# Kernel tuning notes

Hardware: AMD Instinct MI355X
Metric: run time of the kernel (lower is better)

Reference implementation:

```python
import jax, jax.numpy as jnp
import numpy as np

R = 5.0      # cutoff radius (init arg)
N = 4096     # total atoms
B = 8        # number of periodic systems in the batch


def setup_inputs() -> dict:
    key = jax.random.key(0)
    k1, k2, k3 = jax.random.split(key, 3)
    # positions in a ~20 Angstrom box (matches cell scale)
    pos = jax.random.uniform(k1, (N, 3), dtype=jnp.float32) * 20.0
    # sorted per-atom graph ids, as produced by a batched molecular loader
    batch = jnp.sort(jax.random.randint(k2, (N,), 0, B))
    # near-cubic 20A cells with small triclinic perturbation (well-conditioned)
    cell = jnp.eye(3, dtype=jnp.float32) * 20.0 + 0.5 * jax.random.normal(k3, (B, 3, 3), dtype=jnp.float32)
    return {"pos": pos, "cell": cell, "batch": batch}


def reference(pos, cell, batch):
    # Dense, fixed-shape equivalent of RadiusGraph.forward with PBC cell wrap.
    # Original returns dynamically filtered (edge_index, disp); here we return
    # the full [N,N,3] displacement grid (masked to 0 off-graph) plus the
    # boolean edge mask -- same math, jit-compatible static shapes.
    n = pos.shape[0]
    disp = pos[:, None, :] - pos[None, :, :]            # [N,N,3], row i minus col j
    # PBC minimum-image wrap: per edge, cell is taken from the ROW node's graph
    cell_n = cell[batch]                                # [N,3,3]
    inv_cellT = jnp.linalg.inv(jnp.swapaxes(cell_n, 1, 2))   # [N,3,3] = (cell^T)^{-1}
    # scaled = solve(cell^T, disp) vectorized over all pairs
    scaled = jnp.einsum('iab,ijb->ija', inv_cellT, disp)     # [N,N,3]
    disp = disp - jnp.einsum('iab,ijb->ija', cell_n, jnp.round(scaled))
    # edge validity: same graph, no self-loop, within cutoff (after wrap)
    same_graph = batch[:, None] == batch[None, :]
    not_self = ~jnp.eye(n, dtype=bool)
    mask = same_graph & not_self & (jnp.linalg.norm(disp, axis=-1) < R)
    disp = jnp.where(mask[..., None], disp, jnp.zeros((), disp.dtype))
    return disp, mask
```

## Files before the change

### kernel.cpp

```cpp
#include <hip/hip_runtime.h>
#include <math.h>

#define NATOMS 4096
#define R_CUT 5.0f
#define JPT 4
#define BLOCK 256
#define JPB (BLOCK * JPT)
#define IPB 8

typedef float f3 __attribute__((ext_vector_type(3), aligned(4)));

__global__ __launch_bounds__(BLOCK) void radius_graph_kernel(
    const float* __restrict__ pos,
    const float* __restrict__ cell,
    const int*   __restrict__ batch,
    float* __restrict__ disp_out,
    float* __restrict__ mask_out)
{
    const int bid = blockIdx.x;
    const int rg  = bid >> 2;
    const int jc  = bid & 3;
    const int tid = (int)threadIdx.x;

    float pjx[JPT], pjy[JPT], pjz[JPT];
    int   bj[JPT];
    #pragma unroll
    for (int k = 0; k < JPT; ++k) {
        const int j = jc * JPB + k * BLOCK + tid;
        pjx[k] = pos[j * 3 + 0];
        pjy[k] = pos[j * 3 + 1];
        pjz[k] = pos[j * 3 + 2];
        bj[k]  = batch[j];
    }

    const int i0 = rg * IPB;

    #pragma unroll 1
    for (int r = 0; r < IPB; ++r) {
        const int i = i0 + r;

        const int bi = batch[i];
        const float pix = pos[i * 3 + 0];
        const float piy = pos[i * 3 + 1];
        const float piz = pos[i * 3 + 2];

        const float* C = cell + (size_t)bi * 9;
        const float C00 = C[0], C01 = C[1], C02 = C[2];
        const float C10 = C[3], C11 = C[4], C12 = C[5];
        const float C20 = C[6], C21 = C[7], C22 = C[8];
        const float cof00 =  (C11 * C22 - C12 * C21);
        const float cof01 = -(C10 * C22 - C12 * C20);
        const float cof02 =  (C10 * C21 - C11 * C20);
        const float cof10 = -(C01 * C22 - C02 * C21);
        const float cof11 =  (C00 * C22 - C02 * C20);
        const float cof12 = -(C00 * C21 - C01 * C20);
        const float cof20 =  (C01 * C12 - C02 * C11);
        const float cof21 = -(C00 * C12 - C02 * C10);
        const float cof22 =  (C00 * C11 - C01 * C10);
        const float det = C00 * cof00 + C01 * cof01 + C02 * cof02;
        const float id  = 1.0f / det;
        const float A00 = cof00 * id, A01 = cof01 * id, A02 = cof02 * id;
        const float A10 = cof10 * id, A11 = cof11 * id, A12 = cof12 * id;
        const float A20 = cof20 * id, A21 = cof21 * id, A22 = cof22 * id;

        const size_t rowm = (size_t)i * NATOMS;
        const size_t rowd = rowm * 3;

        #pragma unroll
        for (int k = 0; k < JPT; ++k) {
            const int j = jc * JPB + k * BLOCK + tid;
            const float d0 = __fsub_rn(pix, pjx[k]);
            const float d1 = __fsub_rn(piy, pjy[k]);
            const float d2 = __fsub_rn(piz, pjz[k]);

            const float s0 = __fadd_rn(__fadd_rn(__fmul_rn(A00, d0), __fmul_rn(A01, d1)), __fmul_rn(A02, d2));
            const float s1 = __fadd_rn(__fadd_rn(__fmul_rn(A10, d0), __fmul_rn(A11, d1)), __fmul_rn(A12, d2));
            const float s2 = __fadd_rn(__fadd_rn(__fmul_rn(A20, d0), __fmul_rn(A21, d1)), __fmul_rn(A22, d2));

            const float r0 = rintf(s0);
            const float r1 = rintf(s1);
            const float r2 = rintf(s2);

            const float w0 = __fsub_rn(d0, __fadd_rn(__fadd_rn(__fmul_rn(C00, r0), __fmul_rn(C01, r1)), __fmul_rn(C02, r2)));
            const float w1 = __fsub_rn(d1, __fadd_rn(__fadd_rn(__fmul_rn(C10, r0), __fmul_rn(C11, r1)), __fmul_rn(C12, r2)));
            const float w2 = __fsub_rn(d2, __fadd_rn(__fadd_rn(__fmul_rn(C20, r0), __fmul_rn(C21, r1)), __fmul_rn(C22, r2)));

            const float n2 = __fadd_rn(__fadd_rn(__fmul_rn(w0, w0), __fmul_rn(w1, w1)), __fmul_rn(w2, w2));
            const bool m = (bi == bj[k]) && (i != j) && (sqrtf(n2) < R_CUT);

            f3 v;
            v.x = m ? w0 : 0.0f;
            v.y = m ? w1 : 0.0f;
            v.z = m ? w2 : 0.0f;
            *(f3*)(disp_out + rowd + (size_t)j * 3) = v;
            mask_out[rowm + (size_t)j] = m ? 1.0f : 0.0f;
        }
    }
}

extern "C" void kernel_launch(void* const* d_in, const int* in_sizes, int n_in,
                              void* d_out, int out_size, void* d_ws, size_t ws_size,
                              hipStream_t stream) {
    const float* pos   = (const float*)d_in[0];
    const float* cell  = (const float*)d_in[1];
    const int*   batch = (const int*)d_in[2];

    float* disp_out = (float*)d_out;
    float* mask_out = (float*)d_out + (size_t)NATOMS * NATOMS * 3;

    const int blocks = (NATOMS / IPB) * (NATOMS / JPB);
    radius_graph_kernel<<<blocks, BLOCK, 0, stream>>>(pos, cell, batch, disp_out, mask_out);
}
```

Measured before the change: 261.7 us.

## Switch to grid-stride persistent loop over contiguous row tiles

Replaces the fixed 2048-block grid, where each block owned 8 rows by 1024 columns, with a persistent grid of 2048 blocks looping over 256-wide row tiles. Each iteration writes one fully contiguous 256-element chunk of the output, so consecutive blocks stream adjacent memory. The trade-off is that j-atom positions are no longer kept in registers across rows, and the cell inverse is recomputed for every tile, adding loads and ALU work to a store-bound kernel.

```diff
diff --git a/kernel.cpp b/kernel.cpp
--- a/kernel.cpp
+++ b/kernel.cpp
@@ -3,10 +3,10 @@
 
 #define NATOMS 4096
 #define R_CUT 5.0f
-#define JPT 4
 #define BLOCK 256
-#define JPB (BLOCK * JPT)
-#define IPB 8
+#define GRID 2048
+#define TPR (NATOMS / BLOCK)
+#define NTILE (NATOMS * TPR)
 
 typedef float f3 __attribute__((ext_vector_type(3), aligned(4)));
 
@@ -17,27 +17,12 @@
     float* __restrict__ disp_out,
     float* __restrict__ mask_out)
 {
-    const int bid = blockIdx.x;
-    const int rg  = bid >> 2;
-    const int jc  = bid & 3;
     const int tid = (int)threadIdx.x;
 
-    float pjx[JPT], pjy[JPT], pjz[JPT];
-    int   bj[JPT];
-    #pragma unroll
-    for (int k = 0; k < JPT; ++k) {
-        const int j = jc * JPB + k * BLOCK + tid;
-        pjx[k] = pos[j * 3 + 0];
-        pjy[k] = pos[j * 3 + 1];
-        pjz[k] = pos[j * 3 + 2];
-        bj[k]  = batch[j];
-    }
-
-    const int i0 = rg * IPB;
-
-    #pragma unroll 1
-    for (int r = 0; r < IPB; ++r) {
-        const int i = i0 + r;
+    for (int T = (int)blockIdx.x; T < NTILE; T += GRID) {
+        const int i  = T >> 4;
+        const int jb = T & (TPR - 1);
+        const int j  = jb * BLOCK + tid;
 
         const int bi = batch[i];
         const float pix = pos[i * 3 + 0];
@@ -63,38 +48,36 @@
         const float A10 = cof10 * id, A11 = cof11 * id, A12 = cof12 * id;
         const float A20 = cof20 * id, A21 = cof21 * id, A22 = cof22 * id;
 
-        const size_t rowm = (size_t)i * NATOMS;
-        const size_t rowd = rowm * 3;
+        const float pjx = pos[j * 3 + 0];
+        const float pjy = pos[j * 3 + 1];
+        const float pjz = pos[j * 3 + 2];
+        const int   bjv = batch[j];
 
-        #pragma unroll
-        for (int k = 0; k < JPT; ++k) {
-            const int j = jc * JPB + k * BLOCK + tid;
-            const float d0 = __fsub_rn(pix, pjx[k]);
-            const float d1 = __fsub_rn(piy, pjy[k]);
-            const float d2 = __fsub_rn(piz, pjz[k]);
+        const float d0 = __fsub_rn(pix, pjx);
+        const float d1 = __fsub_rn(piy, pjy);
+        const float d2 = __fsub_rn(piz, pjz);
 
-            const float s0 = __fadd_rn(__fadd_rn(__fmul_rn(A00, d0), __fmul_rn(A01, d1)), __fmul_rn(A02, d2));
-            const float s1 = __fadd_rn(__fadd_rn(__fmul_rn(A10, d0), __fmul_rn(A11, d1)), __fmul_rn(A12, d2));
-            const float s2 = __fadd_rn(__fadd_rn(__fmul_rn(A20, d0), __fmul_rn(A21, d1)), __fmul_rn(A22, d2));
+        const float s0 = __fadd_rn(__fadd_rn(__fmul_rn(A00, d0), __fmul_rn(A01, d1)), __fmul_rn(A02, d2));
+        const float s1 = __fadd_rn(__fadd_rn(__fmul_rn(A10, d0), __fmul_rn(A11, d1)), __fmul_rn(A12, d2));
+        const float s2 = __fadd_rn(__fadd_rn(__fmul_rn(A20, d0), __fmul_rn(A21, d1)), __fmul_rn(A22, d2));
 
-            const float r0 = rintf(s0);
-            const float r1 = rintf(s1);
-            const float r2 = rintf(s2);
+        const float r0 = rintf(s0);
+        const float r1 = rintf(s1);
+        const float r2 = rintf(s2);
 
-            const float w0 = __fsub_rn(d0, __fadd_rn(__fadd_rn(__fmul_rn(C00, r0), __fmul_rn(C01, r1)), __fmul_rn(C02, r2)));
-            const float w1 = __fsub_rn(d1, __fadd_rn(__fadd_rn(__fmul_rn(C10, r0), __fmul_rn(C11, r1)), __fmul_rn(C12, r2)));
-            const float w2 = __fsub_rn(d2, __fadd_rn(__fadd_rn(__fmul_rn(C20, r0), __fmul_rn(C21, r1)), __fmul_rn(C22, r2)));
+        const float w0 = __fsub_rn(d0, __fadd_rn(__fadd_rn(__fmul_rn(C00, r0), __fmul_rn(C01, r1)), __fmul_rn(C02, r2)));
+        const float w1 = __fsub_rn(d1, __fadd_rn(__fadd_rn(__fmul_rn(C10, r0), __fmul_rn(C11, r1)), __fmul_rn(C12, r2)));
+        const float w2 = __fsub_rn(d2, __fadd_rn(__fadd_rn(__fmul_rn(C20, r0), __fmul_rn(C21, r1)), __fmul_rn(C22, r2)));
 
-            const float n2 = __fadd_rn(__fadd_rn(__fmul_rn(w0, w0), __fmul_rn(w1, w1)), __fmul_rn(w2, w2));
-            const bool m = (bi == bj[k]) && (i != j) && (sqrtf(n2) < R_CUT);
+        const float n2 = __fadd_rn(__fadd_rn(__fmul_rn(w0, w0), __fmul_rn(w1, w1)), __fmul_rn(w2, w2));
+        const bool m = (bi == bjv) && (i != j) && (sqrtf(n2) < R_CUT);
 
-            f3 v;
-            v.x = m ? w0 : 0.0f;
-            v.y = m ? w1 : 0.0f;
-            v.z = m ? w2 : 0.0f;
-            *(f3*)(disp_out + rowd + (size_t)j * 3) = v;
-            mask_out[rowm + (size_t)j] = m ? 1.0f : 0.0f;
-        }
+        f3 v;
+        v.x = m ? w0 : 0.0f;
+        v.y = m ? w1 : 0.0f;
+        v.z = m ? w2 : 0.0f;
+        *(f3*)(disp_out + (size_t)T * (BLOCK * 3) + (size_t)tid * 3) = v;
+        mask_out[(size_t)T * BLOCK + tid] = m ? 1.0f : 0.0f;
     }
 }
 
@@ -108,6 +91,5 @@
     float* disp_out = (float*)d_out;
     float* mask_out = (float*)d_out + (size_t)NATOMS * NATOMS * 3;
 
-    const int blocks = (NATOMS / IPB) * (NATOMS / JPB);
-    radius_graph_kernel<<<blocks, BLOCK, 0, stream>>>(pos, cell, batch, disp_out, mask_out);
+    radius_graph_kernel<<<GRID, BLOCK, 0, stream>>>(pos, cell, batch, disp_out, mask_out);
 }
```

Result: no change. 262.7 us (+0.4%).
